# Performance work log

Measured on AMD Instinct MI355X. Metric: run time of the kernel, lower is better.

Reference implementation:

```python
import jax, jax.numpy as jnp
import numpy as np

N = 100000   # nodes
E = 1600000  # edges
D = 128      # out_feats
V = 5000     # annotation_size
L = 3        # n_steps SAGE layers


def setup_inputs() -> dict:
    key = jax.random.key(0)
    k0, k1, k2, k3, k4 = jax.random.split(key, 5)
    annotation = jax.random.randint(k0, (N,), 0, V)
    src = jax.random.randint(k1, (E,), 0, N)
    dst = jax.random.randint(k2, (E,), 0, N)
    emb = jax.random.normal(k3, (V, D), dtype=jnp.float32) * 0.02
    Ws = jax.random.normal(k4, (L, D, D), dtype=jnp.float32) / np.sqrt(D).astype(np.float32)
    bs = jnp.zeros((L, D), dtype=jnp.float32)
    return {"annotation": annotation, "src": src, "dst": dst, "emb": emb, "Ws": Ws, "bs": bs}


def reference(annotation, src, dst, emb, Ws, bs):
    # tok_embedding == 2: embedding lookup of node token ids
    h = emb[annotation]                                              # [N, D]
    # in-degree per destination node (constant across layers)
    deg = jax.ops.segment_sum(jnp.ones_like(src, dtype=jnp.float32), dst, num_segments=N)
    inv = 1.0 / (deg + 1.0)                                          # [N]
    # DGL SAGEConv, aggregator_type='gcn', eval mode (feat_drop is identity):
    #   h_neigh = (h_self + sum_{u->v} h_u) / (in_deg + 1); rst = relu(h_neigh @ W + b)
    for l in range(L):
        agg = jax.ops.segment_sum(h[src], dst, num_segments=N)       # [N, D] gather-scatter
        h = jax.nn.relu(((h + agg) * inv[:, None]) @ Ws[l] + bs[l])
    # residual=False -> merged node features are just h ('_merge_on nodes h')
    return h
```

## Files before the change

### kernel.cpp

```cpp
#include <hip/hip_runtime.h>
#include <hip/hip_fp16.h>


#define D 128
#define PBLK 128
#define BSH 7

typedef float f32x4 __attribute__((ext_vector_type(4)));
typedef _Float16 f16x8 __attribute__((ext_vector_type(8)));

__global__ __launch_bounds__(256) void k_hist(
    const int* __restrict__ dst, int* __restrict__ hist,
    int E, int chunk, int nbk) {
    __shared__ int lh[1024];
    int j = blockIdx.x, tid = threadIdx.x;
    for (int i = tid; i < nbk; i += 256) lh[i] = 0;
    __syncthreads();
    int e0 = j * chunk, e1 = min(E, e0 + chunk);
    for (int e = e0 + tid; e < e1; e += 256)
        atomicAdd(&lh[dst[e] >> BSH], 1);
    __syncthreads();
    for (int i = tid; i < nbk; i += 256) hist[(size_t)j * nbk + i] = lh[i];
}

__global__ void k_scan_offs(int* __restrict__ hist, int* __restrict__ tot, int nbk) {
    __shared__ int s[PBLK];
    int b = blockIdx.x, j = threadIdx.x;
    int v = hist[(size_t)j * nbk + b];
    s[j] = v;
    __syncthreads();
    for (int off = 1; off < PBLK; off <<= 1) {
        int x = (j >= off) ? s[j - off] : 0;
        __syncthreads();
        s[j] += x;
        __syncthreads();
    }
    hist[(size_t)j * nbk + b] = s[j] - v;
    if (j == PBLK - 1) tot[b] = s[j];
}

__global__ void k_scan_tot(int* __restrict__ tot, int* __restrict__ row_ptr,
                           int nbk, int N, int E) {
    __shared__ int s[1024];
    int t = threadIdx.x;
    int v = (t < nbk) ? tot[t] : 0;
    s[t] = v;
    __syncthreads();
    for (int off = 1; off < 1024; off <<= 1) {
        int x = (t >= off) ? s[t - off] : 0;
        __syncthreads();
        s[t] += x;
        __syncthreads();
    }
    if (t < nbk) tot[t] = s[t] - v;
    if (t == 0) { tot[nbk] = E; row_ptr[N] = E; }
}

__global__ __launch_bounds__(256) void k_scatter(
    const int* __restrict__ src, const int* __restrict__ dst,
    const int* __restrict__ ann, const int* __restrict__ hist,
    const int* __restrict__ tot, int2* __restrict__ tmp,
    int E, int chunk, int nbk) {
    __shared__ int cur[1024];
    int j = blockIdx.x, tid = threadIdx.x;
    for (int i = tid; i < nbk; i += 256)
        cur[i] = tot[i] + hist[(size_t)j * nbk + i];
    __syncthreads();
    int e0 = j * chunk, e1 = min(E, e0 + chunk);
    for (int e = e0 + tid; e < e1; e += 256) {
        int d = dst[e], s = src[e];
        int p = atomicAdd(&cur[d >> BSH], 1);
        tmp[p] = make_int2(s, ((d & ((1 << BSH) - 1)) << 13) | ann[s]);
    }
}

__global__ __launch_bounds__(256) void k_place(
    const int2* __restrict__ tmp, const int* __restrict__ tot,
    int* __restrict__ row_ptr, int2* __restrict__ eal, int N) {
    __shared__ int cnt[1 << BSH], sc[1 << BSH];
    int b = blockIdx.x, tid = threadIdx.x;
    int base = tot[b], end = tot[b + 1];
    if (tid < (1 << BSH)) cnt[tid] = 0;
    __syncthreads();
    for (int i = base + tid; i < end; i += 256)
        atomicAdd(&cnt[((unsigned)tmp[i].y) >> 13], 1);
    __syncthreads();
    if (tid < (1 << BSH)) sc[tid] = cnt[tid];
    __syncthreads();
    for (int off = 1; off < (1 << BSH); off <<= 1) {
        int x = (tid < (1 << BSH) && tid >= off) ? sc[tid - off] : 0;
        __syncthreads();
        if (tid < (1 << BSH)) sc[tid] += x;
        __syncthreads();
    }
    if (tid < (1 << BSH)) {
        int excl = sc[tid] - cnt[tid];
        int d0 = (b << BSH) + tid;
        if (d0 < N) row_ptr[d0] = base + excl;
        cnt[tid] = excl;
    }
    __syncthreads();
    for (int i = base + tid; i < end; i += 256) {
        int2 w = tmp[i];
        int p = atomicAdd(&cnt[((unsigned)w.y) >> 13], 1);
        eal[base + p] = make_int2(w.x, w.y & 0x1FFF);
    }
}

union H16Chunk { float4 f4; __half2 h2[4]; __half h[8]; };

__global__ void k_h16(const float* __restrict__ x, __half* __restrict__ y, int n8) {
    int i = blockIdx.x * blockDim.x + threadIdx.x;
    if (i >= n8) return;
    const float4* p = (const float4*)x;
    float4 a = p[2 * i], b = p[2 * i + 1];
    H16Chunk u;
    u.h2[0] = __floats2half2_rn(a.x, a.y);
    u.h2[1] = __floats2half2_rn(a.z, a.w);
    u.h2[2] = __floats2half2_rn(b.x, b.y);
    u.h2[3] = __floats2half2_rn(b.z, b.w);
    *(float4*)&y[8 * i] = u.f4;
}

#define XT_LD 136
__global__ __launch_bounds__(256) void k_gemm_mfma(
    const __half* __restrict__ x16, const float* __restrict__ W,
    __half* __restrict__ g16, int n, int ntiles) {
    __shared__ __half Bf[8 * 4 * 64 * 8];
    __shared__ __half Xt[64 * XT_LD];
    int tid = threadIdx.x;
    int lane = tid & 63;
    int wv = tid >> 6;

    for (int idx = tid; idx < 8 * 4 * 64; idx += 256) {
        int l = idx & 63, ks = (idx >> 6) & 3, nt = idx >> 8;
        int kq = (l >> 4) * 8;
        int col = nt * 16 + (l & 15);
        H16Chunk u;
        #pragma unroll
        for (int j = 0; j < 8; j++)
            u.h[j] = __float2half(W[(ks * 32 + kq + j) * 128 + col]);
        *(float4*)&Bf[idx * 8] = u.f4;
    }
    __syncthreads();

    f16x8 breg[8][4];
    #pragma unroll
    for (int nt = 0; nt < 8; nt++)
        #pragma unroll
        for (int ks = 0; ks < 4; ks++)
            breg[nt][ks] = *(f16x8*)&Bf[((nt * 4 + ks) * 64 + lane) * 8];

    int srow = tid >> 2;
    int sc = (tid & 3) * 32;
    int m = lane & 15, quad = lane >> 4;

    for (int tile = blockIdx.x; tile < ntiles; tile += gridDim.x) {
        int row0 = tile * 64;
        __syncthreads();
        {
            int gr = row0 + srow;
            if (gr >= n) gr = n - 1;
            const float4* xp = (const float4*)&x16[(size_t)gr * 128 + sc];
            float4 v0 = xp[0], v1 = xp[1], v2 = xp[2], v3 = xp[3];
            float4* xd = (float4*)&Xt[srow * XT_LD + sc];
            xd[0] = v0; xd[1] = v1; xd[2] = v2; xd[3] = v3;
        }
        __syncthreads();

        f32x4 acc[8];
        #pragma unroll
        for (int nt = 0; nt < 8; nt++) acc[nt] = (f32x4){0.f, 0.f, 0.f, 0.f};
        #pragma unroll
        for (int ks = 0; ks < 4; ks++) {
            f16x8 a = *(f16x8*)&Xt[(wv * 16 + m) * XT_LD + ks * 32 + quad * 8];
            #pragma unroll
            for (int nt = 0; nt < 8; nt++)
                acc[nt] = __builtin_amdgcn_mfma_f32_16x16x32_f16(a, breg[nt][ks], acc[nt], 0, 0, 0);
        }
        __syncthreads();
        #pragma unroll
        for (int nt = 0; nt < 8; nt++)
            #pragma unroll
            for (int r = 0; r < 4; r++)
                Xt[(wv * 16 + quad * 4 + r) * XT_LD + nt * 16 + m] = __float2half(acc[nt][r]);
        __syncthreads();
        {
            int gr = row0 + srow;
            if (gr < n) {
                float4* gp = (float4*)&g16[(size_t)gr * 128 + sc];
                float4* xs = (float4*)&Xt[srow * XT_LD + sc];
                gp[0] = xs[0]; gp[1] = xs[1]; gp[2] = xs[2]; gp[3] = xs[3];
            }
        }
    }
}

template<bool SELY>
__global__ __launch_bounds__(512) void k_agg_gemm(
    const float4* __restrict__ tab, const int* __restrict__ selfidx,
    const int* __restrict__ row_ptr, const int2* __restrict__ eal,
    const float4* __restrict__ bias4, const float* __restrict__ W,
    __half* __restrict__ g16, int n, int ntiles) {
    __shared__ __half Bf[8 * 4 * 64 * 8];
    __shared__ __half Xt[64 * XT_LD];
    int tid = threadIdx.x;
    int lane = tid & 63;
    int wv = tid >> 6;
    int g = lane >> 4;
    int q = lane & 15;

    for (int idx = tid; idx < 8 * 4 * 64; idx += 512) {
        int l = idx & 63, ks = (idx >> 6) & 3, nt = idx >> 8;
        int kq = (l >> 4) * 8;
        int col = nt * 16 + (l & 15);
        H16Chunk u;
        #pragma unroll
        for (int j = 0; j < 8; j++)
            u.h[j] = __float2half(W[(ks * 32 + kq + j) * 128 + col]);
        *(float4*)&Bf[idx * 8] = u.f4;
    }
    __syncthreads();

    int stripe = wv >> 1;
    int ntb = (wv & 1) * 4;
    float4 b0 = bias4[2 * q], b1 = bias4[2 * q + 1];

    #define ACCUM(raw) do { H16Chunk u; u.f4 = (raw);                          \
        float2 t0 = __half22float2(u.h2[0]); acc[0] += t0.x; acc[1] += t0.y;   \
        float2 t1 = __half22float2(u.h2[1]); acc[2] += t1.x; acc[3] += t1.y;   \
        float2 t2 = __half22float2(u.h2[2]); acc[4] += t2.x; acc[5] += t2.y;   \
        float2 t3 = __half22float2(u.h2[3]); acc[6] += t3.x; acc[7] += t3.y; } while (0)
    #define IDX(w) (SELY ? (w).y : (w).x)

    for (int tile = blockIdx.x; tile < ntiles; tile += gridDim.x) {
        int row0 = tile * 64;
        __syncthreads();
        for (int j = 0; j < 8; j++) {
            int r = wv * 8 + j;
            int v = row0 + r;
            int vv = (v < n) ? v : 0;
            int beg = row_ptr[vv];
            int end = (v < n) ? row_ptr[vv + 1] : beg;
            int deg = end - beg;
            float acc[8] = {};
            if (g == 0) {
                int sr = SELY ? selfidx[vv] : vv;
                ACCUM(tab[(size_t)sr * 16 + q]);
            }
            int quads = deg >> 2;
            int p = 0;
            for (; p + 4 <= quads; p += 4) {
                int eb = beg + 4 * p + g;
                int2 w0 = eal[eb + 0], w1 = eal[eb + 4];
                int2 w2 = eal[eb + 8], w3 = eal[eb + 12];
                float4 r0 = tab[(size_t)IDX(w0) * 16 + q];
                float4 r1 = tab[(size_t)IDX(w1) * 16 + q];
                float4 r2 = tab[(size_t)IDX(w2) * 16 + q];
                float4 r3 = tab[(size_t)IDX(w3) * 16 + q];
                ACCUM(r0); ACCUM(r1); ACCUM(r2); ACCUM(r3);
            }
            for (; p < quads; p++) ACCUM(tab[(size_t)IDX(eal[beg + 4 * p + g]) * 16 + q]);
            int tail = deg & 3;
            if (g < tail) ACCUM(tab[(size_t)IDX(eal[beg + 4 * quads + g]) * 16 + q]);

            #pragma unroll
            for (int jj = 0; jj < 8; jj++) {
                acc[jj] += __shfl_down(acc[jj], 16, 64);
                acc[jj] += __shfl_down(acc[jj], 32, 64);
            }
            if (g == 0) {
                float sc = 1.0f / (float)(deg + 1);
                H16Chunk u;
                u.h2[0] = __floats2half2_rn(fmaxf(acc[0] * sc + b0.x, 0.f),
                                            fmaxf(acc[1] * sc + b0.y, 0.f));
                u.h2[1] = __floats2half2_rn(fmaxf(acc[2] * sc + b0.z, 0.f),
                                            fmaxf(acc[3] * sc + b0.w, 0.f));
                u.h2[2] = __floats2half2_rn(fmaxf(acc[4] * sc + b1.x, 0.f),
                                            fmaxf(acc[5] * sc + b1.y, 0.f));
                u.h2[3] = __floats2half2_rn(fmaxf(acc[6] * sc + b1.z, 0.f),
                                            fmaxf(acc[7] * sc + b1.w, 0.f));
                *(float4*)&Xt[r * XT_LD + q * 8] = u.f4;
            }
        }
        __syncthreads();
        f32x4 cacc[4];
        #pragma unroll
        for (int t = 0; t < 4; t++) cacc[t] = (f32x4){0.f, 0.f, 0.f, 0.f};
        #pragma unroll
        for (int ks = 0; ks < 4; ks++) {
            f16x8 a = *(f16x8*)&Xt[(stripe * 16 + q) * XT_LD + ks * 32 + g * 8];
            #pragma unroll
            for (int t = 0; t < 4; t++) {
                f16x8 b = *(f16x8*)&Bf[(((ntb + t) * 4 + ks) * 64 + lane) * 8];
                cacc[t] = __builtin_amdgcn_mfma_f32_16x16x32_f16(a, b, cacc[t], 0, 0, 0);
            }
        }
        __syncthreads();
        #pragma unroll
        for (int t = 0; t < 4; t++)
            #pragma unroll
            for (int r4 = 0; r4 < 4; r4++)
                Xt[(stripe * 16 + g * 4 + r4) * XT_LD + (ntb + t) * 16 + q] =
                    __float2half(cacc[t][r4]);
        __syncthreads();
        {
            int srow = tid >> 3, c = tid & 7;
            int gr = row0 + srow;
            float4 v0 = *(float4*)&Xt[srow * XT_LD + c * 16];
            float4 v1 = *(float4*)&Xt[srow * XT_LD + c * 16 + 8];
            if (gr < n) {
                float4* gp = (float4*)&g16[(size_t)gr * 128 + c * 16];
                gp[0] = v0;
                gp[1] = v1;
            }
        }
    }
    #undef ACCUM
    #undef IDX
}

template<bool SELY, bool OUT32>
__global__ __launch_bounds__(256) void k_agg(
    const float4* __restrict__ tab, const int* __restrict__ selfidx,
    const int* __restrict__ row_ptr, const int2* __restrict__ eal,
    const float4* __restrict__ bias4,
    __half* __restrict__ h16out, float* __restrict__ f32out, int n) {
    int v = blockIdx.x * 4 + (threadIdx.x >> 6);
    int lane = threadIdx.x & 63;
    int g = lane >> 4;
    int q = lane & 15;
    int beg = row_ptr[v], end = row_ptr[v + 1];
    int deg = end - beg;
    float acc[8] = {};

    #define ACCUM(raw) do { H16Chunk u; u.f4 = (raw);                          \
        float2 t0 = __half22float2(u.h2[0]); acc[0] += t0.x; acc[1] += t0.y;   \
        float2 t1 = __half22float2(u.h2[1]); acc[2] += t1.x; acc[3] += t1.y;   \
        float2 t2 = __half22float2(u.h2[2]); acc[4] += t2.x; acc[5] += t2.y;   \
        float2 t3 = __half22float2(u.h2[3]); acc[6] += t3.x; acc[7] += t3.y; } while (0)
    #define IDX(w) (SELY ? (w).y : (w).x)

    if (g == 0) {
        int sr = SELY ? selfidx[v] : v;
        ACCUM(tab[(size_t)sr * 16 + q]);
    }

    int quads = deg >> 2;
    int p = 0;
    for (; p + 4 <= quads; p += 4) {
        int eb = beg + 4 * p + g;
        int2 w0 = eal[eb + 0], w1 = eal[eb + 4], w2 = eal[eb + 8], w3 = eal[eb + 12];
        float4 r0 = tab[(size_t)IDX(w0) * 16 + q], r1 = tab[(size_t)IDX(w1) * 16 + q];
        float4 r2 = tab[(size_t)IDX(w2) * 16 + q], r3 = tab[(size_t)IDX(w3) * 16 + q];
        ACCUM(r0); ACCUM(r1); ACCUM(r2); ACCUM(r3);
    }
    for (; p < quads; p++) ACCUM(tab[(size_t)IDX(eal[beg + 4 * p + g]) * 16 + q]);
    int tail = deg & 3;
    if (g < tail) ACCUM(tab[(size_t)IDX(eal[beg + 4 * quads + g]) * 16 + q]);
    #undef ACCUM
    #undef IDX

    #pragma unroll
    for (int j = 0; j < 8; j++) {
        acc[j] += __shfl_down(acc[j], 16, 64);
        acc[j] += __shfl_down(acc[j], 32, 64);
    }
    if (g == 0) {
        float sc = 1.0f / (float)(deg + 1);
        float4 b0 = bias4[2 * q], b1 = bias4[2 * q + 1];
        float o[8];
        o[0] = fmaxf(acc[0] * sc + b0.x, 0.f);
        o[1] = fmaxf(acc[1] * sc + b0.y, 0.f);
        o[2] = fmaxf(acc[2] * sc + b0.z, 0.f);
        o[3] = fmaxf(acc[3] * sc + b0.w, 0.f);
        o[4] = fmaxf(acc[4] * sc + b1.x, 0.f);
        o[5] = fmaxf(acc[5] * sc + b1.y, 0.f);
        o[6] = fmaxf(acc[6] * sc + b1.z, 0.f);
        o[7] = fmaxf(acc[7] * sc + b1.w, 0.f);
        if (!OUT32) {
            H16Chunk u;
            u.h2[0] = __floats2half2_rn(o[0], o[1]);
            u.h2[1] = __floats2half2_rn(o[2], o[3]);
            u.h2[2] = __floats2half2_rn(o[4], o[5]);
            u.h2[3] = __floats2half2_rn(o[6], o[7]);
            *(float4*)&h16out[(size_t)v * 128 + q * 8] = u.f4;
        } else {
            f32x4 a = {o[0], o[1], o[2], o[3]};
            f32x4 b = {o[4], o[5], o[6], o[7]};
            __builtin_nontemporal_store(a, (f32x4*)&f32out[(size_t)v * 128 + q * 8]);
            __builtin_nontemporal_store(b, (f32x4*)&f32out[(size_t)v * 128 + q * 8 + 4]);
        }
    }
}

extern "C" void kernel_launch(void* const* d_in, const int* in_sizes, int n_in,
                              void* d_out, int out_size, void* d_ws, size_t ws_size,
                              hipStream_t stream) {
    const int*   ann = (const int*)d_in[0];
    const int*   src = (const int*)d_in[1];
    const int*   dst = (const int*)d_in[2];
    const float* emb = (const float*)d_in[3];
    const float* Ws  = (const float*)d_in[4];
    const float* bs  = (const float*)d_in[5];
    float* out = (float*)d_out;

    const int N = in_sizes[0];
    const int E = in_sizes[1];
    const int V = in_sizes[3] / D;
    const int NT64 = (N + 63) / 64;
    const int VT64 = (V + 63) / 64;
    const int NBK  = (N + (1 << BSH) - 1) >> BSH;
    const int CHK  = (E + PBLK - 1) / PBLK;

    int*  deg     = (int*)d_ws;
    int*  row_ptr = deg + N;
    int*  bsum    = row_ptr + ((N + 1 + 3) & ~3);
    int2* eal     = (int2*)(bsum + 512);
    __half* hA16  = (__half*)(eal + E);
    __half* gB16  = hA16 + (size_t)N * D;
    __half* embW16= gB16 + (size_t)N * D;
    __half* emb16 = embW16 + (size_t)V * D;
    int2* tmp  = (int2*)hA16;
    int*  hist = (int*)gB16;
    int*  tot  = hist + (size_t)PBLK * NBK;

    k_h16<<<(V * D / 8 + 255) / 256, 256, 0, stream>>>(emb, emb16, V * D / 8);
    k_gemm_mfma<<<VT64, 256, 0, stream>>>(emb16, Ws, embW16, V, VT64);

    k_hist<<<PBLK, 256, 0, stream>>>(dst, hist, E, CHK, NBK);
    k_scan_offs<<<NBK, PBLK, 0, stream>>>(hist, tot, NBK);
    k_scan_tot<<<1, 1024, 0, stream>>>(tot, row_ptr, NBK, N, E);
    k_scatter<<<PBLK, 256, 0, stream>>>(src, dst, ann, hist, tot, tmp, E, CHK, NBK);
    k_place<<<NBK, 256, 0, stream>>>(tmp, tot, row_ptr, eal, N);

    k_agg_gemm<true><<<NT64, 512, 0, stream>>>(
        (const float4*)embW16, ann, row_ptr, eal, (const float4*)bs,
        Ws + (size_t)D * D, gB16, N, NT64);

    k_agg_gemm<false><<<NT64, 512, 0, stream>>>(
        (const float4*)gB16, nullptr, row_ptr, eal, (const float4*)(bs + D),
        Ws + (size_t)2 * D * D, hA16, N, NT64);

    k_agg<false, true><<<N / 4, 256, 0, stream>>>(
        (const float4*)hA16, nullptr, row_ptr, eal, (const float4*)(bs + 2 * D),
        nullptr, out, N);
}
```

Baseline: 455.9 us.

## Precompute fp16 weight fragments once and balance rows via an LDS cursor

A new small kernel converts the layer-2 and layer-3 weights into MFMA B-fragment layout in fp16, once per forward pass. Previously every block of the fused aggregate+GEMM kernel redid that conversion with strided global reads and kept a 32KB LDS copy. The fused kernel now reads B fragments straight from global memory, where they should stay L2-resident. It drops the Bf LDS buffer and adds launch bounds asking for more resident blocks, and waves claim destination rows from a shared atomic cursor instead of a fixed 8 rows each, to even out skewed degrees. The cost is uncached global B loads inside the MFMA loop and reuse of the deg workspace region for the fragments.

```diff
diff --git a/kernel.cpp b/kernel.cpp
--- a/kernel.cpp
+++ b/kernel.cpp
@@ -122,6 +122,21 @@
     *(float4*)&y[8 * i] = u.f4;
 }
 
+__global__ void k_wfrag(const float* __restrict__ Ws, __half* __restrict__ Wf) {
+    const float* W = Ws + (size_t)(blockIdx.x + 1) * D * D;
+    __half* o = Wf + (size_t)blockIdx.x * 2048 * 8;
+    for (int idx = threadIdx.x; idx < 2048; idx += 256) {
+        int l = idx & 63, ks = (idx >> 6) & 3, nt = idx >> 8;
+        int kq = (l >> 4) * 8;
+        int col = nt * 16 + (l & 15);
+        H16Chunk u;
+        #pragma unroll
+        for (int j = 0; j < 8; j++)
+            u.h[j] = __float2half(W[(ks * 32 + kq + j) * 128 + col]);
+        *(float4*)&o[idx * 8] = u.f4;
+    }
+}
+
 #define XT_LD 136
 __global__ __launch_bounds__(256) void k_gemm_mfma(
     const __half* __restrict__ x16, const float* __restrict__ W,
@@ -197,30 +212,18 @@
 }
 
 template<bool SELY>
-__global__ __launch_bounds__(512) void k_agg_gemm(
+__global__ __launch_bounds__(512, 8) void k_agg_gemm(
     const float4* __restrict__ tab, const int* __restrict__ selfidx,
     const int* __restrict__ row_ptr, const int2* __restrict__ eal,
-    const float4* __restrict__ bias4, const float* __restrict__ W,
+    const float4* __restrict__ bias4, const __half* __restrict__ Wf,
     __half* __restrict__ g16, int n, int ntiles) {
-    __shared__ __half Bf[8 * 4 * 64 * 8];
     __shared__ __half Xt[64 * XT_LD];
+    __shared__ int cursor;
     int tid = threadIdx.x;
     int lane = tid & 63;
     int wv = tid >> 6;
     int g = lane >> 4;
     int q = lane & 15;
-
-    for (int idx = tid; idx < 8 * 4 * 64; idx += 512) {
-        int l = idx & 63, ks = (idx >> 6) & 3, nt = idx >> 8;
-        int kq = (l >> 4) * 8;
-        int col = nt * 16 + (l & 15);
-        H16Chunk u;
-        #pragma unroll
-        for (int j = 0; j < 8; j++)
-            u.h[j] = __float2half(W[(ks * 32 + kq + j) * 128 + col]);
-        *(float4*)&Bf[idx * 8] = u.f4;
-    }
-    __syncthreads();
 
     int stripe = wv >> 1;
     int ntb = (wv & 1) * 4;
@@ -235,9 +238,13 @@
 
     for (int tile = blockIdx.x; tile < ntiles; tile += gridDim.x) {
         int row0 = tile * 64;
-        __syncthreads();
-        for (int j = 0; j < 8; j++) {
-            int r = wv * 8 + j;
+        if (tid == 0) cursor = 0;
+        __syncthreads();
+        for (;;) {
+            int r;
+            if (lane == 0) r = atomicAdd(&cursor, 1);
+            r = __shfl(r, 0, 64);
+            if (r >= 64) break;
             int v = row0 + r;
             int vv = (v < n) ? v : 0;
             int beg = row_ptr[vv];
@@ -292,7 +299,7 @@
             f16x8 a = *(f16x8*)&Xt[(stripe * 16 + q) * XT_LD + ks * 32 + g * 8];
             #pragma unroll
             for (int t = 0; t < 4; t++) {
-                f16x8 b = *(f16x8*)&Bf[(((ntb + t) * 4 + ks) * 64 + lane) * 8];
+                f16x8 b = *(const f16x8*)&Wf[(((ntb + t) * 4 + ks) * 64 + lane) * 8];
                 cacc[t] = __builtin_amdgcn_mfma_f32_16x16x32_f16(a, b, cacc[t], 0, 0, 0);
             }
         }
@@ -424,8 +431,11 @@
     int2* tmp  = (int2*)hA16;
     int*  hist = (int*)gB16;
     int*  tot  = hist + (size_t)PBLK * NBK;
+    __half* Wf2 = (__half*)deg;
+    __half* Wf3 = Wf2 + 2048 * 8;
 
     k_h16<<<(V * D / 8 + 255) / 256, 256, 0, stream>>>(emb, emb16, V * D / 8);
+    k_wfrag<<<2, 256, 0, stream>>>(Ws, Wf2);
     k_gemm_mfma<<<VT64, 256, 0, stream>>>(emb16, Ws, embW16, V, VT64);
 
     k_hist<<<PBLK, 256, 0, stream>>>(dst, hist, E, CHK, NBK);
@@ -436,11 +446,11 @@
 
     k_agg_gemm<true><<<NT64, 512, 0, stream>>>(
         (const float4*)embW16, ann, row_ptr, eal, (const float4*)bs,
-        Ws + (size_t)D * D, gB16, N, NT64);
+        Wf2, gB16, N, NT64);
 
     k_agg_gemm<false><<<NT64, 512, 0, stream>>>(
         (const float4*)gB16, nullptr, row_ptr, eal, (const float4*)(bs + D),
-        Ws + (size_t)2 * D * D, hA16, N, NT64);
+        Wf3, hA16, N, NT64);
 
     k_agg<false, true><<<N / 4, 256, 0, stream>>>(
         (const float4*)hA16, nullptr, row_ptr, eal, (const float4*)(bs + 2 * D),
```

Result: slower. 540.3 us (+18.5%).
